# Kernel optimization log

Hardware: AMD Instinct MI355X
Metric: run time of the kernel (lower is better)

## Reference

```python
import jax, jax.numpy as jnp
import numpy as np

B = 2097152  # flattened batch of 3x3 rotation matrices

def setup_inputs() -> dict:
    key = jax.random.key(0)
    k1, k2 = jax.random.split(key)
    # scale by 0.1 so cos=(trace(m1 m2^T)-1)/2 stays strictly inside (-1,1)
    pred_rot = jax.random.normal(k1, (B, 3, 3), dtype=jnp.float32) * 0.1
    gt_rot = jax.random.normal(k2, (B, 3, 3), dtype=jnp.float32) * 0.1
    return {"pred_rot": pred_rot, "gt_rot": gt_rot}

def reference(pred_rot, gt_rot):
    m1 = pred_rot.reshape(-1, 3, 3)
    m2 = gt_rot.reshape(-1, 3, 3)
    # trace(m1 @ m2^T) == sum(m1 * m2) elementwise -> avoid the bmm
    cos = (jnp.einsum('bij,bij->b', m1, m2) - 1.0) * 0.5
    cos = jnp.clip(cos, -1.0, 1.0)  # min with +1, max with -1
    theta = jnp.arccos(cos)
    return jnp.mean(theta)  # reduction='mean'
```

## Files before the change

kernel.cpp:

```cpp
#include <hip/hip_runtime.h>
#include <math.h>


#define TPB 256
#define NBLOCKS 2048
#define MPW 256
#define MPB 1024
#define W4_PER_WAVE 576
#define LDSF_PER_WAVE 2304

__global__ __launch_bounds__(TPB) void geo_kernel(
    const float* __restrict__ a, const float* __restrict__ b,
    float* __restrict__ out, float invM, int M)
{
    __shared__ float prod[4 * LDSF_PER_WAVE];
    __shared__ float wsum[TPB / 64];

    const int tid  = threadIdx.x;
    const int lane = tid & 63;
    const int wv   = tid >> 6;
    float* lp = prod + wv * LDSF_PER_WAVE;

    float sum = 0.0f;
    const long long NT = (long long)M / MPB;

    for (long long t = blockIdx.x; t < NT; t += gridDim.x) {
        const long long base4 = t * (9LL * MPB / 4) + wv * W4_PER_WAVE + lane;
        const float4* __restrict__ pa = (const float4*)a + base4;
        const float4* __restrict__ pb = (const float4*)b + base4;
        const float4 A0 = pa[0],   A1 = pa[64],  A2 = pa[128],
                     A3 = pa[192], A4 = pa[256], A5 = pa[320],
                     A6 = pa[384], A7 = pa[448], A8 = pa[512];
        const float4 B0 = pb[0],   B1 = pb[64],  B2 = pb[128],
                     B3 = pb[192], B4 = pb[256], B5 = pb[320],
                     B6 = pb[384], B7 = pb[448], B8 = pb[512];

        #define PK(k)                                                       \
        {                                                                   \
            float4 p;                                                       \
            p.x = A##k.x * B##k.x; p.y = A##k.y * B##k.y;                   \
            p.z = A##k.z * B##k.z; p.w = A##k.w * B##k.w;                   \
            *(float4*)&lp[4 * (64 * (k) + lane)] = p;                       \
        }
        PK(0) PK(1) PK(2) PK(3) PK(4) PK(5) PK(6) PK(7) PK(8)
        #undef PK

        asm volatile("s_waitcnt lgkmcnt(0)" ::: "memory");

        #pragma unroll
        for (int q = 0; q < 4; ++q) {
            const float* r = lp + 9 * (64 * q + lane);
            float d = ((r[0] + r[1]) + (r[2] + r[3])) +
                      ((r[4] + r[5]) + (r[6] + r[7])) + r[8];
            float cv = fminf(1.0f, fmaxf(-1.0f, (d - 1.0f) * 0.5f));
            sum += acosf(cv);
        }

        asm volatile("s_waitcnt lgkmcnt(0)" ::: "memory");
    }

    {
        const long long gid    = (long long)blockIdx.x * TPB + tid;
        const long long stride = (long long)gridDim.x * TPB;
        for (long long m = NT * MPB + gid; m < M; m += stride) {
            float d = 0.0f;
            #pragma unroll
            for (int j = 0; j < 9; ++j)
                d = fmaf(a[m * 9 + j], b[m * 9 + j], d);
            float cv = fminf(1.0f, fmaxf(-1.0f, (d - 1.0f) * 0.5f));
            sum += acosf(cv);
        }
    }

    #pragma unroll
    for (int off = 32; off > 0; off >>= 1)
        sum += __shfl_down(sum, off, 64);
    if ((tid & 63) == 0) wsum[tid >> 6] = sum;
    __syncthreads();
    if (tid == 0) {
        float s = 0.0f;
        #pragma unroll
        for (int i = 0; i < TPB / 64; ++i) s += wsum[i];
        atomicAdd(out, s * invM);
    }
}

extern "C" void kernel_launch(void* const* d_in, const int* in_sizes, int n_in,
                              void* d_out, int out_size, void* d_ws, size_t ws_size,
                              hipStream_t stream) {
    const float* a = (const float*)d_in[0];
    const float* b = (const float*)d_in[1];
    float* out = (float*)d_out;

    const int n = in_sizes[0];
    const int M = n / 9;

    hipMemsetAsync(out, 0, (size_t)out_size * sizeof(float), stream);
    geo_kernel<<<NBLOCKS, TPB, 0, stream>>>(a, b, out, 1.0f / (float)M, M);
}
```

Baseline: 169.0 us.

## Replace LDS transpose with quad-lane shuffle reduction over 4-matrix groups

Drops the shared-memory staging buffer that regrouped elementwise products into per-matrix rows. Instead, each group of 4 lanes handles 4 matrices (36 floats = 9 float4s). Each lane loads two private float4s plus the shared ninth, forms partial dot products, and combines them with xor shuffles, so each lane ends up with one matrix's trace. This removes LDS writes, reads and waits, but adds redundant loads of the shared float4, lane-dependent selects and 8 shuffles per iteration. Loads within a quad are also less contiguous across the wave.

```diff
diff --git a/kernel.cpp b/kernel.cpp
--- a/kernel.cpp
+++ b/kernel.cpp
@@ -4,71 +4,72 @@
 
 #define TPB 256
 #define NBLOCKS 2048
-#define MPW 256
-#define MPB 1024
-#define W4_PER_WAVE 576
-#define LDSF_PER_WAVE 2304
 
 __global__ __launch_bounds__(TPB) void geo_kernel(
     const float* __restrict__ a, const float* __restrict__ b,
     float* __restrict__ out, float invM, int M)
 {
-    __shared__ float prod[4 * LDSF_PER_WAVE];
     __shared__ float wsum[TPB / 64];
-
-    const int tid  = threadIdx.x;
-    const int lane = tid & 63;
-    const int wv   = tid >> 6;
-    float* lp = prod + wv * LDSF_PER_WAVE;
+    const int tid = threadIdx.x;
+    const int q   = tid & 3;
 
     float sum = 0.0f;
-    const long long NT = (long long)M / MPB;
 
-    for (long long t = blockIdx.x; t < NT; t += gridDim.x) {
-        const long long base4 = t * (9LL * MPB / 4) + wv * W4_PER_WAVE + lane;
-        const float4* __restrict__ pa = (const float4*)a + base4;
-        const float4* __restrict__ pb = (const float4*)b + base4;
-        const float4 A0 = pa[0],   A1 = pa[64],  A2 = pa[128],
-                     A3 = pa[192], A4 = pa[256], A5 = pa[320],
-                     A6 = pa[384], A7 = pa[448], A8 = pa[512];
-        const float4 B0 = pb[0],   B1 = pb[64],  B2 = pb[128],
-                     B3 = pb[192], B4 = pb[256], B5 = pb[320],
-                     B6 = pb[384], B7 = pb[448], B8 = pb[512];
+    const long long G    = (long long)M >> 2;
+    const long long Q0   = (long long)blockIdx.x * (TPB / 4) + (tid >> 2);
+    const long long Qstr = (long long)gridDim.x * (TPB / 4);
 
-        #define PK(k)                                                       \
-        {                                                                   \
-            float4 p;                                                       \
-            p.x = A##k.x * B##k.x; p.y = A##k.y * B##k.y;                   \
-            p.z = A##k.z * B##k.z; p.w = A##k.w * B##k.w;                   \
-            *(float4*)&lp[4 * (64 * (k) + lane)] = p;                       \
-        }
-        PK(0) PK(1) PK(2) PK(3) PK(4) PK(5) PK(6) PK(7) PK(8)
-        #undef PK
+    const float4* __restrict__ a4 = (const float4*)a;
+    const float4* __restrict__ b4 = (const float4*)b;
 
-        asm volatile("s_waitcnt lgkmcnt(0)" ::: "memory");
+    for (long long Q = Q0; Q < G; Q += Qstr) {
+        const float4* __restrict__ pa = a4 + 9 * Q;
+        const float4* __restrict__ pb = b4 + 9 * Q;
+        const float4 A0 = pa[q], A1 = pa[4 + q], A2 = pa[8];
+        const float4 B0 = pb[q], B1 = pb[4 + q], B2 = pb[8];
 
-        #pragma unroll
-        for (int q = 0; q < 4; ++q) {
-            const float* r = lp + 9 * (64 * q + lane);
-            float d = ((r[0] + r[1]) + (r[2] + r[3])) +
-                      ((r[4] + r[5]) + (r[6] + r[7])) + r[8];
-            float cv = fminf(1.0f, fmaxf(-1.0f, (d - 1.0f) * 0.5f));
-            sum += acosf(cv);
-        }
+        float4 t0, t1;
+        t0.x = A0.x * B0.x; t0.y = A0.y * B0.y;
+        t0.z = A0.z * B0.z; t0.w = A0.w * B0.w;
+        t1.x = A1.x * B1.x; t1.y = A1.y * B1.y;
+        t1.z = A1.z * B1.z; t1.w = A1.w * B1.w;
 
-        asm volatile("s_waitcnt lgkmcnt(0)" ::: "memory");
+        const float c01 = t0.x + t0.y;
+        const float T0  = (c01 + t0.z) + t0.w;
+        const float d01 = t1.x + t1.y;
+        const float T1  = (d01 + t1.z) + t1.w;
+
+        float P0 = (q == 3) ? 0.0f : ((q == 2) ? t0.x : T0);
+        float P1 = (q == 0) ? d01  : ((q == 1) ? 0.0f
+                   : ((q == 2) ? (T0 - t0.x) : T0));
+        float P2 = (q == 0) ? (T1 - d01) : ((q == 1) ? T1
+                   : ((q == 2) ? (T1 - t1.w) : 0.0f));
+        float P3 = (q == 2) ? t1.w : ((q == 3) ? T1 : 0.0f);
+
+        P0 += __shfl_xor(P0, 1, 64); P0 += __shfl_xor(P0, 2, 64);
+        P1 += __shfl_xor(P1, 1, 64); P1 += __shfl_xor(P1, 2, 64);
+        P2 += __shfl_xor(P2, 1, 64); P2 += __shfl_xor(P2, 2, 64);
+        P3 += __shfl_xor(P3, 1, 64); P3 += __shfl_xor(P3, 2, 64);
+
+        const float u0 = A2.x * B2.x, u1 = A2.y * B2.y;
+        const float u2 = A2.z * B2.z, u3 = A2.w * B2.w;
+        const float dl2 = (u0 + u1) + (u2 + u3);
+
+        const float d = (q == 0) ? P0 : (q == 1) ? P1
+                      : (q == 2) ? P2 : (P3 + dl2);
+        const float cv = fminf(1.0f, fmaxf(-1.0f, (d - 1.0f) * 0.5f));
+        sum += acosf(cv);
     }
 
     {
         const long long gid    = (long long)blockIdx.x * TPB + tid;
         const long long stride = (long long)gridDim.x * TPB;
-        for (long long m = NT * MPB + gid; m < M; m += stride) {
+        for (long long m = 4 * G + gid; m < M; m += stride) {
             float d = 0.0f;
             #pragma unroll
             for (int j = 0; j < 9; ++j)
                 d = fmaf(a[m * 9 + j], b[m * 9 + j], d);
-            float cv = fminf(1.0f, fmaxf(-1.0f, (d - 1.0f) * 0.5f));
-            sum += acosf(cv);
+            sum += acosf(fminf(1.0f, fmaxf(-1.0f, (d - 1.0f) * 0.5f)));
         }
     }
 
```

After: 171.3 us. About the same (+1.4%).
